# Kernel tuning notes

Hardware: AMD Instinct MI355X
Metric: run time of the kernel (lower is better)

The kernel has to match this reference:

```python
import jax, jax.numpy as jnp
import numpy as np

INPUT_SIZE = 34
HIDDEN = 4
NUM_CLASSES = 3
B, T = 4096, 200


def setup_inputs() -> dict:
    key = jax.random.key(0)
    ks = jax.random.split(key, 8)
    k = 1.0 / np.sqrt(HIDDEN)  # torch default uniform init bound
    u = lambda kk, shape: jax.random.uniform(kk, shape, jnp.float32, -k, k)
    x = jax.random.normal(ks[0], (B, T, INPUT_SIZE), jnp.float32)
    W_ih = u(ks[1], (4 * HIDDEN, INPUT_SIZE))   # gate order: i, f, g, o
    W_hh = u(ks[2], (4 * HIDDEN, HIDDEN))
    b_ih = u(ks[3], (4 * HIDDEN,))
    b_hh = u(ks[4], (4 * HIDDEN,))
    W_fc = u(ks[5], (NUM_CLASSES, HIDDEN))
    b_fc = u(ks[6], (NUM_CLASSES,))
    return {"x": x, "W_ih": W_ih, "W_hh": W_hh, "b_ih": b_ih,
            "b_hh": b_hh, "W_fc": W_fc, "b_fc": b_fc}


def reference(x, W_ih, W_hh, b_ih, b_hh, W_fc, b_fc):
    Bsz = x.shape[0]
    H = W_hh.shape[1]
    # Precompute input contributions for all timesteps: [B, T, 4H]
    x_gates = jnp.einsum('btd,gd->btg', x, W_ih) + b_ih + b_hh
    x_gates = jnp.swapaxes(x_gates, 0, 1)  # [T, B, 4H] for scan

    def step(carry, xg_t):
        h, c = carry
        gates = xg_t + h @ W_hh.T          # [B, 4H]
        i, f, g, o = jnp.split(gates, 4, axis=-1)
        i = jax.nn.sigmoid(i)
        f = jax.nn.sigmoid(f)
        g = jnp.tanh(g)
        o = jax.nn.sigmoid(o)
        c = f * c + i * g
        h = o * jnp.tanh(c)
        return (h, c), None

    h0 = jnp.zeros((Bsz, H), x.dtype)
    c0 = jnp.zeros((Bsz, H), x.dtype)
    (h_last, _), _ = jax.lax.scan(step, (h0, c0), x_gates)
    # dropout is identity in eval mode
    return h_last @ W_fc.T + b_fc  # [B, num_classes]
```

## Files before the change

### kernel.cpp

```cpp
#include <hip/hip_runtime.h>
#include <hip/hip_fp16.h>

#define B_SZ 4096
#define T_SZ 200
#define IN_SZ 34
#define TILES (B_SZ * T_SZ / 64)
#define XG_BLOCKS 1024
#define WAVES_TOTAL (XG_BLOCKS * 2)
#define WT_FLOATS 560

__device__ __forceinline__ float sigf(float x) {
    return 1.0f / (1.0f + __expf(-x));
}
__device__ __forceinline__ float tanh_f(float x) {
    return 2.0f / (1.0f + __expf(-2.0f * x)) - 1.0f;
}

__device__ __forceinline__ float quad_bcast0(float v) {
    int s = __float_as_int(v);
    return __int_as_float(__builtin_amdgcn_update_dpp(s, s, 0x00, 0xf, 0xf, true));
}
__device__ __forceinline__ float quad_bcast1(float v) {
    int s = __float_as_int(v);
    return __int_as_float(__builtin_amdgcn_update_dpp(s, s, 0x55, 0xf, 0xf, true));
}
__device__ __forceinline__ float quad_bcast2(float v) {
    int s = __float_as_int(v);
    return __int_as_float(__builtin_amdgcn_update_dpp(s, s, 0xAA, 0xf, 0xf, true));
}
__device__ __forceinline__ float quad_bcast3(float v) {
    int s = __float_as_int(v);
    return __int_as_float(__builtin_amdgcn_update_dpp(s, s, 0xFF, 0xf, 0xf, true));
}

typedef const __attribute__((address_space(1))) unsigned int* gas_t;
typedef __attribute__((address_space(3))) unsigned int* las_t;

__global__ __launch_bounds__(64) void prep_kernel(
    const float* __restrict__ W_ih, const float* __restrict__ b_ih,
    const float* __restrict__ b_hh, float* __restrict__ wt) {
  for (int i = threadIdx.x; i < WT_FLOATS; i += 64) {
    if (i < 544) {
      int k = i >> 4, g = i & 15;
      wt[i] = W_ih[g * IN_SZ + k];
    } else {
      wt[i] = b_ih[i - 544] + b_hh[i - 544];
    }
  }
}

__global__ __launch_bounds__(128) void xgates_kernel(
    const float* __restrict__ x, const float* __restrict__ wt,
    __half* __restrict__ xg) {
  __shared__ float xs[2 * 2 * 64 * IN_SZ];
  const int lane = threadIdx.x & 63;
  const int wv = threadIdx.x >> 6;
  float* buf0 = &xs[wv * 2 * 64 * IN_SZ];
  float* buf1 = buf0 + 64 * IN_SZ;
  const int gw = blockIdx.x * 2 + wv;

  float bias[16];
  #pragma unroll
  for (int g = 0; g < 16; ++g) bias[g] = wt[544 + g];

  auto issue = [&](int tile, float* buf) {
    const float4* src = reinterpret_cast<const float4*>(x + (size_t)tile * 64 * IN_SZ);
    char* l = reinterpret_cast<char*>(buf);
    #pragma unroll
    for (int i = 0; i < 8; ++i)
      __builtin_amdgcn_global_load_lds((gas_t)(src + i * 64 + lane),
                                       (las_t)(l + i * 1024), 16, 0, 0);
    if (lane < 32)
      __builtin_amdgcn_global_load_lds((gas_t)(src + 512 + lane),
                                       (las_t)(l + 8192), 16, 0, 0);
  };

  int tile = gw;
  if (tile < TILES) issue(tile, buf0);
  int cur = 0;
  #pragma unroll 1
  for (; tile < TILES; tile += WAVES_TOTAL) {
    int nxt = tile + WAVES_TOTAL;
    if (nxt < TILES) {
      issue(nxt, cur ? buf0 : buf1);
      asm volatile("s_waitcnt vmcnt(9)" ::: "memory");
    } else {
      asm volatile("s_waitcnt vmcnt(0)" ::: "memory");
    }
    __builtin_amdgcn_sched_barrier(0);

    const float* buf = cur ? buf1 : buf0;
    float xr[IN_SZ];
    const float2* rp = reinterpret_cast<const float2*>(buf + lane * IN_SZ);
    #pragma unroll
    for (int k = 0; k < IN_SZ / 2; ++k) {
      float2 v = rp[k];
      xr[2 * k] = v.x;
      xr[2 * k + 1] = v.y;
    }
    float acc[16];
    #pragma unroll
    for (int g = 0; g < 16; ++g) acc[g] = bias[g];
    #pragma unroll
    for (int k = 0; k < IN_SZ; ++k) {
      #pragma unroll
      for (int g = 0; g < 16; ++g)
        acc[g] = fmaf(xr[k], wt[k * 16 + g], acc[g]);
    }
    union {
      __half2 h[8];
      int4 v[2];
    } u;
    #pragma unroll
    for (int j = 0; j < 4; ++j) {
      u.h[2 * j + 0] = __floats2half2_rn(acc[0 + j], acc[4 + j]);
      u.h[2 * j + 1] = __floats2half2_rn(acc[8 + j], acc[12 + j]);
    }
    size_t row = (size_t)tile * 64 + lane;
    int4* op = reinterpret_cast<int4*>(xg + row * 16);
    op[0] = u.v[0];
    op[1] = u.v[1];
    cur ^= 1;
  }
}

#define U_SZ 10
__global__ __launch_bounds__(64) void lstm_scan(
    const __half* __restrict__ xg, const float* __restrict__ W_hh,
    const float* __restrict__ W_fc, const float* __restrict__ b_fc,
    float* __restrict__ out) {
  int tid = blockIdx.x * 64 + threadIdx.x;
  int b = tid >> 2;
  int j = tid & 3;
  float Wi[4], Wf[4], Wg[4], Wo[4];
  #pragma unroll
  for (int k = 0; k < 4; ++k) {
    Wi[k] = W_hh[(0 + j) * 4 + k];
    Wf[k] = W_hh[(4 + j) * 4 + k];
    Wg[k] = W_hh[(8 + j) * 4 + k];
    Wo[k] = W_hh[(12 + j) * 4 + k];
  }
  float h[4] = {0.f, 0.f, 0.f, 0.f};
  float c = 0.f;

  auto step = [&](uint2 w) {
    union {
      uint2 u;
      __half2 h2[2];
    } v;
    v.u = w;
    float2 p01 = __half22float2(v.h2[0]);
    float2 p23 = __half22float2(v.h2[1]);
    float pi = p01.x, pf = p01.y, pg = p23.x, po = p23.y;
    #pragma unroll
    for (int k = 0; k < 4; ++k) {
      pi = fmaf(Wi[k], h[k], pi);
      pf = fmaf(Wf[k], h[k], pf);
      pg = fmaf(Wg[k], h[k], pg);
      po = fmaf(Wo[k], h[k], po);
    }
    float iv = sigf(pi);
    float fv = sigf(pf);
    float gv = tanh_f(pg);
    float ov = sigf(po);
    c = fmaf(fv, c, iv * gv);
    float hj = ov * tanh_f(c);
    h[0] = quad_bcast0(hj);
    h[1] = quad_bcast1(hj);
    h[2] = quad_bcast2(hj);
    h[3] = quad_bcast3(hj);
  };

  const uint2* xp = reinterpret_cast<const uint2*>(xg) + (size_t)b * (T_SZ * 4) + j;
  uint2 bufA[U_SZ], bufB[U_SZ];
  #pragma unroll
  for (int u = 0; u < U_SZ; ++u) bufA[u] = xp[4 * u];

  #pragma unroll 1
  for (int blk = 0; blk < 20; blk += 2) {
    const uint2* p1 = xp + (size_t)(blk + 1) * (4 * U_SZ);
    #pragma unroll
    for (int u = 0; u < U_SZ; ++u) bufB[u] = p1[4 * u];
    #pragma unroll
    for (int u = 0; u < U_SZ; ++u) step(bufA[u]);
    if (blk + 2 < 20) {
      const uint2* p2 = xp + (size_t)(blk + 2) * (4 * U_SZ);
      #pragma unroll
      for (int u = 0; u < U_SZ; ++u) bufA[u] = p2[4 * u];
    }
    #pragma unroll
    for (int u = 0; u < U_SZ; ++u) step(bufB[u]);
  }

  if (j < 3) {
    float acc = b_fc[j];
    #pragma unroll
    for (int k = 0; k < 4; ++k) acc = fmaf(W_fc[j * 4 + k], h[k], acc);
    out[b * 3 + j] = acc;
  }
}

__global__ __launch_bounds__(256) void lstm_fused(
    const float* __restrict__ x, const float* __restrict__ W_ih,
    const float* __restrict__ W_hh, const float* __restrict__ b_ih,
    const float* __restrict__ b_hh, const float* __restrict__ W_fc,
    const float* __restrict__ b_fc, float* __restrict__ out) {
  __shared__ float Ws[16 * IN_SZ];
  for (int i = threadIdx.x; i < 16 * IN_SZ; i += 256) Ws[i] = W_ih[i];
  __syncthreads();
  int tid = blockIdx.x * 256 + threadIdx.x;
  int b = tid >> 2;
  int j = tid & 3;
  float bi = b_ih[0 + j] + b_hh[0 + j];
  float bf = b_ih[4 + j] + b_hh[4 + j];
  float bg = b_ih[8 + j] + b_hh[8 + j];
  float bo = b_ih[12 + j] + b_hh[12 + j];
  float Wi[4], Wf[4], Wg[4], Wo[4];
  #pragma unroll
  for (int k = 0; k < 4; ++k) {
    Wi[k] = W_hh[(0 + j) * 4 + k];
    Wf[k] = W_hh[(4 + j) * 4 + k];
    Wg[k] = W_hh[(8 + j) * 4 + k];
    Wo[k] = W_hh[(12 + j) * 4 + k];
  }
  float h[4] = {0.f, 0.f, 0.f, 0.f};
  float c = 0.f;
  const float2* xp = reinterpret_cast<const float2*>(x + (size_t)b * T_SZ * IN_SZ);
  int lbase = (threadIdx.x & 63) & ~3;
  for (int t = 0; t < T_SZ; ++t) {
    float xr[IN_SZ];
    #pragma unroll
    for (int k = 0; k < IN_SZ / 2; ++k) {
      float2 v = xp[(size_t)t * (IN_SZ / 2) + k];
      xr[2 * k] = v.x;
      xr[2 * k + 1] = v.y;
    }
    float pi = bi, pf = bf, pg = bg, po = bo;
    #pragma unroll
    for (int k = 0; k < IN_SZ; ++k) {
      pi = fmaf(xr[k], Ws[(0 + j) * IN_SZ + k], pi);
      pf = fmaf(xr[k], Ws[(4 + j) * IN_SZ + k], pf);
      pg = fmaf(xr[k], Ws[(8 + j) * IN_SZ + k], pg);
      po = fmaf(xr[k], Ws[(12 + j) * IN_SZ + k], po);
    }
    #pragma unroll
    for (int k = 0; k < 4; ++k) {
      pi = fmaf(Wi[k], h[k], pi);
      pf = fmaf(Wf[k], h[k], pf);
      pg = fmaf(Wg[k], h[k], pg);
      po = fmaf(Wo[k], h[k], po);
    }
    float iv = sigf(pi);
    float fv = sigf(pf);
    float gv = tanh_f(pg);
    float ov = sigf(po);
    c = fmaf(fv, c, iv * gv);
    float hj = ov * tanh_f(c);
    h[0] = __shfl(hj, lbase + 0);
    h[1] = __shfl(hj, lbase + 1);
    h[2] = __shfl(hj, lbase + 2);
    h[3] = __shfl(hj, lbase + 3);
  }
  if (j < 3) {
    float acc = b_fc[j];
    #pragma unroll
    for (int k = 0; k < 4; ++k) acc = fmaf(W_fc[j * 4 + k], h[k], acc);
    out[b * 3 + j] = acc;
  }
}

extern "C" void kernel_launch(void* const* d_in, const int* in_sizes, int n_in,
                              void* d_out, int out_size, void* d_ws, size_t ws_size,
                              hipStream_t stream) {
  const float* x    = (const float*)d_in[0];
  const float* W_ih = (const float*)d_in[1];
  const float* W_hh = (const float*)d_in[2];
  const float* b_ih = (const float*)d_in[3];
  const float* b_hh = (const float*)d_in[4];
  const float* W_fc = (const float*)d_in[5];
  const float* b_fc = (const float*)d_in[6];
  float* out = (float*)d_out;

  const size_t xg_off = 4096;
  const size_t need = xg_off + (size_t)B_SZ * T_SZ * 16 * sizeof(__half);
  if (ws_size >= need) {
    float* wt = (float*)d_ws;
    __half* xg = (__half*)((char*)d_ws + xg_off);
    hipLaunchKernelGGL(prep_kernel, dim3(1), dim3(64), 0, stream,
                       W_ih, b_ih, b_hh, wt);
    hipLaunchKernelGGL(xgates_kernel, dim3(XG_BLOCKS), dim3(128), 0, stream,
                       x, wt, xg);
    hipLaunchKernelGGL(lstm_scan, dim3(B_SZ * 4 / 64), dim3(64), 0, stream,
                       xg, W_hh, W_fc, b_fc, out);
  } else {
    hipLaunchKernelGGL(lstm_fused, dim3(B_SZ * 4 / 256), dim3(256), 0, stream,
                       x, W_ih, W_hh, b_ih, b_hh, W_fc, b_fc, out);
  }
}
```

Before: 82.99 us.

## Transpose xg layout per hidden unit and prefetch with inline-asm dwordx4 loads

The gate-projection kernel now writes xg in a [batch][hidden j][time] layout, so each lane in the scan reads a contiguous run of timesteps. The scan kernel issues 16-byte global loads in batches of ten through inline asm, covering two timesteps per load, into two register buffers, and uses explicit vmcnt waits to overlap loads with the recurrence. This is meant to cut load instruction count and latency exposure in the serial scan. The cost is scattered 8-byte stores in the producer kernel and hand-managed waitcnt logic that must match the load issue order.

```diff
diff --git a/kernel.cpp b/kernel.cpp
--- a/kernel.cpp
+++ b/kernel.cpp
@@ -107,24 +107,36 @@
       for (int g = 0; g < 16; ++g)
         acc[g] = fmaf(xr[k], wt[k * 16 + g], acc[g]);
     }
-    union {
-      __half2 h[8];
-      int4 v[2];
-    } u;
+    unsigned r = (unsigned)tile * 64u + (unsigned)lane;
+    unsigned bb = r / 200u;
+    unsigned tt = r - bb * 200u;
+    uint2* xg2 = reinterpret_cast<uint2*>(xg);
+    size_t base = (size_t)bb * 800u + tt;
     #pragma unroll
     for (int j = 0; j < 4; ++j) {
-      u.h[2 * j + 0] = __floats2half2_rn(acc[0 + j], acc[4 + j]);
-      u.h[2 * j + 1] = __floats2half2_rn(acc[8 + j], acc[12 + j]);
-    }
-    size_t row = (size_t)tile * 64 + lane;
-    int4* op = reinterpret_cast<int4*>(xg + row * 16);
-    op[0] = u.v[0];
-    op[1] = u.v[1];
+      union { __half2 h[2]; uint2 v; } u;
+      u.h[0] = __floats2half2_rn(acc[0 + j], acc[4 + j]);
+      u.h[1] = __floats2half2_rn(acc[8 + j], acc[12 + j]);
+      xg2[base + (size_t)j * 200u] = u.v;
+    }
     cur ^= 1;
   }
 }
 
-#define U_SZ 10
+#define LD 10
+#define ISSUE(p_, buf_)                                                        \
+  do {                                                                         \
+    _Pragma("unroll") for (int u_ = 0; u_ < LD; ++u_)                          \
+        asm volatile("global_load_dwordx4 %0, %1, off"                         \
+                     : "=v"(buf_[u_])                                          \
+                     : "v"((p_) + u_ * 16));                                   \
+  } while (0)
+#define WAITV(n_)                                                              \
+  do {                                                                         \
+    asm volatile("s_waitcnt vmcnt(" #n_ ")" ::: "memory");                     \
+    __builtin_amdgcn_sched_barrier(0);                                         \
+  } while (0)
+
 __global__ __launch_bounds__(64) void lstm_scan(
     const __half* __restrict__ xg, const float* __restrict__ W_hh,
     const float* __restrict__ W_fc, const float* __restrict__ b_fc,
@@ -143,14 +155,12 @@
   float h[4] = {0.f, 0.f, 0.f, 0.f};
   float c = 0.f;
 
-  auto step = [&](uint2 w) {
-    union {
-      uint2 u;
-      __half2 h2[2];
-    } v;
-    v.u = w;
-    float2 p01 = __half22float2(v.h2[0]);
-    float2 p23 = __half22float2(v.h2[1]);
+  auto step = [&](unsigned lo, unsigned hi) {
+    union { unsigned u; __half2 h2; } a, bb;
+    a.u = lo;
+    bb.u = hi;
+    float2 p01 = __half22float2(a.h2);
+    float2 p23 = __half22float2(bb.h2);
     float pi = p01.x, pf = p01.y, pg = p23.x, po = p23.y;
     #pragma unroll
     for (int k = 0; k < 4; ++k) {
@@ -171,25 +181,41 @@
     h[3] = quad_bcast3(hj);
   };
 
-  const uint2* xp = reinterpret_cast<const uint2*>(xg) + (size_t)b * (T_SZ * 4) + j;
-  uint2 bufA[U_SZ], bufB[U_SZ];
-  #pragma unroll
-  for (int u = 0; u < U_SZ; ++u) bufA[u] = xp[4 * u];
+  const char* base = reinterpret_cast<const char*>(xg) +
+                     (size_t)b * 6400 + (size_t)j * 1600;
+  uint4 A[LD], Bb[LD];
+
+  ISSUE(base, A);
+  ISSUE(base + 160, Bb);
 
   #pragma unroll 1
-  for (int blk = 0; blk < 20; blk += 2) {
-    const uint2* p1 = xp + (size_t)(blk + 1) * (4 * U_SZ);
-    #pragma unroll
-    for (int u = 0; u < U_SZ; ++u) bufB[u] = p1[4 * u];
-    #pragma unroll
-    for (int u = 0; u < U_SZ; ++u) step(bufA[u]);
-    if (blk + 2 < 20) {
-      const uint2* p2 = xp + (size_t)(blk + 2) * (4 * U_SZ);
-      #pragma unroll
-      for (int u = 0; u < U_SZ; ++u) bufA[u] = p2[4 * u];
-    }
-    #pragma unroll
-    for (int u = 0; u < U_SZ; ++u) step(bufB[u]);
+  for (int p = 0; p < 4; ++p) {
+    WAITV(10);
+    #pragma unroll
+    for (int u = 0; u < LD; ++u) {
+      step(A[u].x, A[u].y);
+      step(A[u].z, A[u].w);
+    }
+    ISSUE(base + (size_t)(2 * p + 2) * 160, A);
+    WAITV(10);
+    #pragma unroll
+    for (int u = 0; u < LD; ++u) {
+      step(Bb[u].x, Bb[u].y);
+      step(Bb[u].z, Bb[u].w);
+    }
+    ISSUE(base + (size_t)(2 * p + 3) * 160, Bb);
+  }
+  WAITV(10);
+  #pragma unroll
+  for (int u = 0; u < LD; ++u) {
+    step(A[u].x, A[u].y);
+    step(A[u].z, A[u].w);
+  }
+  WAITV(0);
+  #pragma unroll
+  for (int u = 0; u < LD; ++u) {
+    step(Bb[u].x, Bb[u].y);
+    step(Bb[u].z, Bb[u].w);
   }
 
   if (j < 3) {
```

After: 84.23 us. Within noise of the previous version (+1.5%).

## Simplify xgates to one row per thread and transpose xg layout per lane

Applied to the files above, without the earlier changes.

Drops the persistent double-buffered LDS-staged xgates kernel in favour of a one-thread-per-row grid that loads x directly with float2 reads. It also changes the xg layout so each scan lane's gate values sit contiguously along time ([b][j][t]), which makes the scan's per-thread loads contiguous. The cost is uncoalesced strided x reads (136-byte row stride per lane) and scattered 8-byte stores in xgates, traded for simpler code and better scan-side locality.

```diff
diff --git a/kernel.cpp b/kernel.cpp
--- a/kernel.cpp
+++ b/kernel.cpp
@@ -4,9 +4,6 @@
 #define B_SZ 4096
 #define T_SZ 200
 #define IN_SZ 34
-#define TILES (B_SZ * T_SZ / 64)
-#define XG_BLOCKS 1024
-#define WAVES_TOTAL (XG_BLOCKS * 2)
 #define WT_FLOATS 560
 
 __device__ __forceinline__ float sigf(float x) {
@@ -32,9 +29,6 @@
     int s = __float_as_int(v);
     return __int_as_float(__builtin_amdgcn_update_dpp(s, s, 0xFF, 0xf, 0xf, true));
 }
-
-typedef const __attribute__((address_space(1))) unsigned int* gas_t;
-typedef __attribute__((address_space(3))) unsigned int* las_t;
 
 __global__ __launch_bounds__(64) void prep_kernel(
     const float* __restrict__ W_ih, const float* __restrict__ b_ih,
@@ -49,78 +43,38 @@
   }
 }
 
-__global__ __launch_bounds__(128) void xgates_kernel(
+__global__ __launch_bounds__(256) void xgates_kernel(
     const float* __restrict__ x, const float* __restrict__ wt,
     __half* __restrict__ xg) {
-  __shared__ float xs[2 * 2 * 64 * IN_SZ];
-  const int lane = threadIdx.x & 63;
-  const int wv = threadIdx.x >> 6;
-  float* buf0 = &xs[wv * 2 * 64 * IN_SZ];
-  float* buf1 = buf0 + 64 * IN_SZ;
-  const int gw = blockIdx.x * 2 + wv;
-
-  float bias[16];
-  #pragma unroll
-  for (int g = 0; g < 16; ++g) bias[g] = wt[544 + g];
-
-  auto issue = [&](int tile, float* buf) {
-    const float4* src = reinterpret_cast<const float4*>(x + (size_t)tile * 64 * IN_SZ);
-    char* l = reinterpret_cast<char*>(buf);
-    #pragma unroll
-    for (int i = 0; i < 8; ++i)
-      __builtin_amdgcn_global_load_lds((gas_t)(src + i * 64 + lane),
-                                       (las_t)(l + i * 1024), 16, 0, 0);
-    if (lane < 32)
-      __builtin_amdgcn_global_load_lds((gas_t)(src + 512 + lane),
-                                       (las_t)(l + 8192), 16, 0, 0);
-  };
-
-  int tile = gw;
-  if (tile < TILES) issue(tile, buf0);
-  int cur = 0;
-  #pragma unroll 1
-  for (; tile < TILES; tile += WAVES_TOTAL) {
-    int nxt = tile + WAVES_TOTAL;
-    if (nxt < TILES) {
-      issue(nxt, cur ? buf0 : buf1);
-      asm volatile("s_waitcnt vmcnt(9)" ::: "memory");
-    } else {
-      asm volatile("s_waitcnt vmcnt(0)" ::: "memory");
-    }
-    __builtin_amdgcn_sched_barrier(0);
-
-    const float* buf = cur ? buf1 : buf0;
-    float xr[IN_SZ];
-    const float2* rp = reinterpret_cast<const float2*>(buf + lane * IN_SZ);
-    #pragma unroll
-    for (int k = 0; k < IN_SZ / 2; ++k) {
-      float2 v = rp[k];
-      xr[2 * k] = v.x;
-      xr[2 * k + 1] = v.y;
-    }
-    float acc[16];
-    #pragma unroll
-    for (int g = 0; g < 16; ++g) acc[g] = bias[g];
-    #pragma unroll
-    for (int k = 0; k < IN_SZ; ++k) {
-      #pragma unroll
-      for (int g = 0; g < 16; ++g)
-        acc[g] = fmaf(xr[k], wt[k * 16 + g], acc[g]);
-    }
-    union {
-      __half2 h[8];
-      int4 v[2];
-    } u;
-    #pragma unroll
-    for (int j = 0; j < 4; ++j) {
-      u.h[2 * j + 0] = __floats2half2_rn(acc[0 + j], acc[4 + j]);
-      u.h[2 * j + 1] = __floats2half2_rn(acc[8 + j], acc[12 + j]);
-    }
-    size_t row = (size_t)tile * 64 + lane;
-    int4* op = reinterpret_cast<int4*>(xg + row * 16);
-    op[0] = u.v[0];
-    op[1] = u.v[1];
-    cur ^= 1;
+  int row = blockIdx.x * 256 + threadIdx.x;
+  float xr[IN_SZ];
+  const float2* xp = reinterpret_cast<const float2*>(x + (size_t)row * IN_SZ);
+  #pragma unroll
+  for (int k = 0; k < IN_SZ / 2; ++k) {
+    float2 v = xp[k];
+    xr[2 * k] = v.x;
+    xr[2 * k + 1] = v.y;
+  }
+  float acc[16];
+  #pragma unroll
+  for (int g = 0; g < 16; ++g) acc[g] = wt[544 + g];
+  #pragma unroll
+  for (int k = 0; k < IN_SZ; ++k) {
+    #pragma unroll
+    for (int g = 0; g < 16; ++g)
+      acc[g] = fmaf(xr[k], wt[k * 16 + g], acc[g]);
+  }
+  unsigned r = (unsigned)row;
+  unsigned bb = r / 200u;
+  unsigned tt = r - bb * 200u;
+  uint2* xg2 = reinterpret_cast<uint2*>(xg);
+  size_t base = (size_t)bb * 800u + tt;
+  #pragma unroll
+  for (int j = 0; j < 4; ++j) {
+    union { __half2 h[2]; uint2 v; } u;
+    u.h[0] = __floats2half2_rn(acc[0 + j], acc[4 + j]);
+    u.h[1] = __floats2half2_rn(acc[8 + j], acc[12 + j]);
+    xg2[base + (size_t)j * 200u] = u.v;
   }
 }
 
@@ -171,22 +125,23 @@
     h[3] = quad_bcast3(hj);
   };
 
-  const uint2* xp = reinterpret_cast<const uint2*>(xg) + (size_t)b * (T_SZ * 4) + j;
+  const uint2* xp = reinterpret_cast<const uint2*>(xg) +
+                    (size_t)b * 800 + (size_t)j * 200;
   uint2 bufA[U_SZ], bufB[U_SZ];
   #pragma unroll
-  for (int u = 0; u < U_SZ; ++u) bufA[u] = xp[4 * u];
+  for (int u = 0; u < U_SZ; ++u) bufA[u] = xp[u];
 
   #pragma unroll 1
   for (int blk = 0; blk < 20; blk += 2) {
-    const uint2* p1 = xp + (size_t)(blk + 1) * (4 * U_SZ);
-    #pragma unroll
-    for (int u = 0; u < U_SZ; ++u) bufB[u] = p1[4 * u];
+    const uint2* p1 = xp + (size_t)(blk + 1) * U_SZ;
+    #pragma unroll
+    for (int u = 0; u < U_SZ; ++u) bufB[u] = p1[u];
     #pragma unroll
     for (int u = 0; u < U_SZ; ++u) step(bufA[u]);
     if (blk + 2 < 20) {
-      const uint2* p2 = xp + (size_t)(blk + 2) * (4 * U_SZ);
+      const uint2* p2 = xp + (size_t)(blk + 2) * U_SZ;
       #pragma unroll
-      for (int u = 0; u < U_SZ; ++u) bufA[u] = p2[4 * u];
+      for (int u = 0; u < U_SZ; ++u) bufA[u] = p2[u];
     }
     #pragma unroll
     for (int u = 0; u < U_SZ; ++u) step(bufB[u]);
@@ -288,7 +243,7 @@
     __half* xg = (__half*)((char*)d_ws + xg_off);
     hipLaunchKernelGGL(prep_kernel, dim3(1), dim3(64), 0, stream,
                        W_ih, b_ih, b_hh, wt);
-    hipLaunchKernelGGL(xgates_kernel, dim3(XG_BLOCKS), dim3(128), 0, stream,
+    hipLaunchKernelGGL(xgates_kernel, dim3(B_SZ * T_SZ / 256), dim3(256), 0, stream,
                        x, wt, xg);
     hipLaunchKernelGGL(lstm_scan, dim3(B_SZ * 4 / 64), dim3(64), 0, stream,
                        xg, W_hh, W_fc, b_fc, out);
```

New measurement: 101.4 us. 1.22x slower.
